# Kernel tuning notes

Hardware: AMD Instinct MI355X
Metric: run time of the kernel (lower is better)

The kernel has to match this reference:

```python
import jax, jax.numpy as jnp
import numpy as np

K = 20            # neighbors
C = 21            # num_classes
P = 16            # patch_size
NROWS = 14        # img_size // patch_size
H = NROWS * P     # 224
TEMP = 1.0        # temperature


def setup_inputs() -> dict:
    key = jax.random.key(0)
    k1, k2, k3 = jax.random.split(key, 3)
    test_feature = jax.random.normal(k1, (8, 196, 384), dtype=jnp.float32)
    train_features = jax.random.normal(k2, (384, 50000), dtype=jnp.float32)
    train_labels = jax.random.randint(k3, (256, 50000), 0, C, dtype=jnp.int32)
    return {"test_feature": test_feature, "train_features": train_features,
            "train_labels": train_labels}


def reference(test_feature, train_features, train_labels):
    bs = test_feature.shape[0]
    # similarity: [bs, num_patches, N_train]
    sim = jnp.einsum('bpd,dn->bpn', test_feature, train_features)
    sim_k, idx = jax.lax.top_k(sim, K)              # [bs, 196, K]
    # gather neighbor patch labels: train_labels [P^2, N] -> [bs, 196, K, P^2]
    nb = train_labels.T[idx]
    # make_grid with nrow=NROWS, padding=0: assemble patches into [bs, K, H, H]
    nb = nb.reshape(bs, NROWS, NROWS, K, P, P)
    nb = nb.transpose(0, 3, 1, 4, 2, 5).reshape(bs, K, H, H)
    nb = nb.transpose(0, 2, 3, 1)                   # [bs, H, H, K]
    # weighted majority vote: nearest-upsample similarities 14x14 -> 224x224
    w = sim_k.reshape(bs, NROWS, NROWS, K)
    w = jnp.repeat(jnp.repeat(w, P, axis=1), P, axis=2)   # [bs, H, H, K]
    w = jax.nn.softmax(w / TEMP, axis=-1)
    # one-hot vote expressed as scatter-add over classes (same math, no
    # [bs,H,H,K,C] materialization)
    rows = jnp.arange(bs * H * H)
    vote = jnp.zeros((bs * H * H, C), dtype=w.dtype)
    vote = vote.at[rows[:, None], nb.reshape(bs * H * H, K)].add(
        w.reshape(bs * H * H, K))
    vote = vote.reshape(bs, H, H, C)
    pred = jnp.argmax(vote, axis=-1)                # [bs, H, H] int
    return pred
```

## Files before the change

kernel.cpp:

```cpp
#include <hip/hip_runtime.h>
#include <float.h>

#define N_TRAIN 50000
#define NPAD    50176
#define NBLK    392
#define MPAD    1664
#define DDIM    384
#define M_ROWS  1568
#define KNN     20
#define K2      24
#define SELMAX  64
#define NCLS    21
#define CAPBUF  768
#define CBMAX   256

typedef __attribute__((ext_vector_type(8))) short bf16x8;
typedef __attribute__((ext_vector_type(4))) float f32x4;

#define GLOAD_LDS16(gp, lp) \
  __builtin_amdgcn_global_load_lds((const __attribute__((address_space(1))) void*)(gp), \
                                   (__attribute__((address_space(3))) void*)(lp), 16, 0, 0)

static __device__ __forceinline__ unsigned short f2bf(float f) {
  unsigned int u = __float_as_uint(f);
  unsigned int r = (u + 0x7fffu + ((u >> 16) & 1u)) >> 16;
  return (unsigned short)r;
}
static __device__ __forceinline__ unsigned int flip32(unsigned int u) {
  return (u & 0x80000000u) ? ~u : (u | 0x80000000u);
}

__global__ __launch_bounds__(256) void transpose_labels(const int* __restrict__ labels,
                                                        unsigned char* __restrict__ labT) {
  __shared__ int tile[64][65];
  const int t  = threadIdx.x;
  const int c0 = blockIdx.x * 64;
  const int r0 = blockIdx.y * 64;
#pragma unroll
  for (int i = 0; i < 16; ++i) {
    int idx = i * 256 + t;
    int r = idx >> 6, c = idx & 63;
    int cc = c0 + c;
    tile[r][c] = (cc < N_TRAIN) ? labels[(size_t)(r0 + r) * N_TRAIN + cc] : 0;
  }
  __syncthreads();
#pragma unroll
  for (int i = 0; i < 16; ++i) {
    int idx = i * 256 + t;
    int c = idx >> 6, r = idx & 63;
    int cc = c0 + c;
    if (cc < N_TRAIN) labT[(size_t)cc * 256 + r0 + r] = (unsigned char)tile[r][c];
  }
}

__global__ __launch_bounds__(256) void conv_bf16A(const float* __restrict__ test,
                                                  unsigned short* __restrict__ bf16A) {
  int idx = blockIdx.x * 256 + threadIdx.x;
  if (idx >= MPAD * DDIM) return;
  int row = idx / DDIM;
  bf16A[idx] = (row < M_ROWS) ? f2bf(test[idx]) : (unsigned short)0;
}

__global__ __launch_bounds__(256) void trans_train_fused(const float* __restrict__ train,
                                                         unsigned short* __restrict__ bhT,
                                                         float* __restrict__ trainT) {
  __shared__ float tile[64][65];
  const int t  = threadIdx.x;
  const int c0 = blockIdx.x * 64;
  const int r0 = blockIdx.y * 64;
#pragma unroll
  for (int i = 0; i < 16; ++i) {
    int idx = i * 256 + t;
    int r = idx >> 6, c = idx & 63;
    int cc = c0 + c;
    tile[r][c] = (cc < N_TRAIN) ? train[(size_t)(r0 + r) * N_TRAIN + cc] : 0.f;
  }
  __syncthreads();
#pragma unroll
  for (int i = 0; i < 16; ++i) {
    int idx = i * 256 + t;
    int c = idx >> 6, r = idx & 63;
    int cc = c0 + c;
    float v = tile[r][c];
    bhT[(size_t)cc * DDIM + r0 + r] = f2bf(v);
    if (cc < N_TRAIN) trainT[(size_t)cc * DDIM + r0 + r] = v;
  }
}

__global__ __launch_bounds__(256) void mfma_gemm(const unsigned short* __restrict__ bf16A,
                                                 const unsigned short* __restrict__ bhT,
                                                 unsigned short* __restrict__ keybuf,
                                                 unsigned short* __restrict__ blkmax) {
  __shared__ unsigned short lds[16384];
  const int t = threadIdx.x;

  const int flat = blockIdx.x;
  const int wrk  = (flat & 7) * 637 + (flat >> 3);
  const int nblk = wrk / 13, mblk = wrk % 13;
  const int m0 = mblk * 128, n0 = nblk * 128;

  const int wid = t >> 6, lane = t & 63;
  const int wr = wid >> 1, wc = wid & 1;
  const int l15 = lane & 15, l4 = lane >> 4;
  const int srow  = lane >> 3;
  const int sslot = (lane & 7) ^ srow;

  f32x4 acc[4][4];
  const f32x4 zero = {0.f, 0.f, 0.f, 0.f};
#pragma unroll
  for (int f = 0; f < 4; ++f)
#pragma unroll
    for (int n = 0; n < 4; ++n) acc[f][n] = zero;

  for (int ks = 0; ks < DDIM / 64; ++ks) {
    __syncthreads();
#pragma unroll
    for (int j = 0; j < 4; ++j) {
      int seg  = wid * 4 + j;
      int arow = seg * 8 + srow;
      GLOAD_LDS16(bf16A + (size_t)(m0 + arow) * DDIM + ks * 64 + sslot * 8,
                  &lds[seg * 512]);
      GLOAD_LDS16(bhT + (size_t)(n0 + arow) * DDIM + ks * 64 + sslot * 8,
                  &lds[8192 + seg * 512]);
    }
    __syncthreads();
#pragma unroll
    for (int k2 = 0; k2 < 2; ++k2) {
      bf16x8 a[4], b[4];
#pragma unroll
      for (int f = 0; f < 4; ++f) {
        int row = wr * 64 + f * 16 + l15;
        int kel = (k2 * 32 + l4 * 8) ^ ((row & 7) << 3);
        a[f] = *(bf16x8*)&lds[row * 64 + kel];
      }
#pragma unroll
      for (int n = 0; n < 4; ++n) {
        int row = wc * 64 + n * 16 + l15;
        int kel = (k2 * 32 + l4 * 8) ^ ((row & 7) << 3);
        b[n] = *(bf16x8*)&lds[8192 + row * 64 + kel];
      }
#pragma unroll
      for (int f = 0; f < 4; ++f)
#pragma unroll
        for (int n = 0; n < 4; ++n)
          acc[f][n] = __builtin_amdgcn_mfma_f32_16x16x32_bf16(a[f], b[n], acc[f][n], 0, 0, 0);
    }
  }

  __syncthreads();
#pragma unroll
  for (int f = 0; f < 4; ++f) {
#pragma unroll
    for (int n = 0; n < 4; ++n) {
      const int col = wc * 64 + n * 16 + l15;
#pragma unroll
      for (int r = 0; r < 4; ++r) {
        const int row = wr * 64 + f * 16 + l4 * 4 + r;
        unsigned int k16 = flip32(__float_as_uint(acc[f][n][r])) >> 16;
        lds[row * 128 + (col ^ ((row & 15) << 3))] = (unsigned short)k16;
      }
    }
  }
  __syncthreads();

  const bool boundary = (n0 + 128 > N_TRAIN);
#pragma unroll
  for (int i = 0; i < 8; ++i) {
    int idx = i * 256 + t;
    int row = idx >> 4;
    int c8  = (idx & 15) * 8;
    uint4 v = *(uint4*)&lds[row * 128 + (c8 ^ ((row & 15) << 3))];
    if (boundary) {
      int nv = N_TRAIN - (n0 + c8);
      v.x &= ((0 < nv) ? 0x0000FFFFu : 0u) | ((1 < nv) ? 0xFFFF0000u : 0u);
      v.y &= ((2 < nv) ? 0x0000FFFFu : 0u) | ((3 < nv) ? 0xFFFF0000u : 0u);
      v.z &= ((4 < nv) ? 0x0000FFFFu : 0u) | ((5 < nv) ? 0xFFFF0000u : 0u);
      v.w &= ((6 < nv) ? 0x0000FFFFu : 0u) | ((7 < nv) ? 0xFFFF0000u : 0u);
    }
    unsigned int mx = v.x & 0xFFFFu;
    mx = max(mx, v.x >> 16); mx = max(mx, v.y & 0xFFFFu); mx = max(mx, v.y >> 16);
    mx = max(mx, v.z & 0xFFFFu); mx = max(mx, v.z >> 16);
    mx = max(mx, v.w & 0xFFFFu); mx = max(mx, v.w >> 16);
    mx = max(mx, (unsigned int)__shfl_xor((int)mx, 1));
    mx = max(mx, (unsigned int)__shfl_xor((int)mx, 2));
    mx = max(mx, (unsigned int)__shfl_xor((int)mx, 4));
    mx = max(mx, (unsigned int)__shfl_xor((int)mx, 8));
    if ((lane & 15) == 0) blkmax[(size_t)(m0 + row) * NBLK + nblk] = (unsigned short)mx;
    if (m0 + row < M_ROWS)
      *(uint4*)&keybuf[(size_t)(m0 + row) * NPAD + n0 + c8] = v;
  }
}

__global__ __launch_bounds__(256) void select_all(const unsigned short* __restrict__ keybuf,
                                                  const unsigned short* __restrict__ blkmax,
                                                  int* __restrict__ selCols,
                                                  int* __restrict__ selCnt) {
  const int t = threadIdx.x, m = blockIdx.x;
  __shared__ unsigned short bm[NBLK];
  __shared__ int clist[CBMAX];
  __shared__ int ccnt;
  __shared__ unsigned int smax[256];
  __shared__ unsigned int sbuf[CAPBUF];
  __shared__ short srk[CAPBUF];
  __shared__ unsigned int scnt, sTauA, sTau;
  __shared__ int sC2;

  if (t == 0) { ccnt = 0; scnt = 0u; sC2 = 0; }
  for (int i = t; i < NBLK; i += 256) bm[i] = blkmax[(size_t)m * NBLK + i];
  __syncthreads();

  for (int i = t; i < NBLK; i += 256) {
    unsigned short v = bm[i];
    int cgt = 0;
    for (int j = 0; j < NBLK; ++j) cgt += (bm[j] > v) ? 1 : 0;
    if (cgt < K2) { int p = atomicAdd(&ccnt, 1); if (p < CBMAX) clist[p] = i; }
  }
  __syncthreads();
  const int CB = min(ccnt, CBMAX);
  const int TOT = CB * 128;

  unsigned int tmx = 0u;
  for (int i = t; i < TOT; i += 256) {
    int col = clist[i >> 7] * 128 + (i & 127);
    unsigned int k = keybuf[(size_t)m * NPAD + col];
    if (k > tmx) tmx = k;
  }
  smax[t] = (tmx << 8) | (unsigned int)(255 - t);
  __syncthreads();
  {
    unsigned int myc = smax[t];
    int rnk = 0;
    for (int j = 0; j < 256; ++j) rnk += (smax[j] > myc) ? 1 : 0;
    if (rnk == K2 - 1) sTauA = myc >> 8;
  }
  __syncthreads();
  const unsigned int tauB = sTauA;

  for (int i = t; i < TOT; i += 256) {
    int col = clist[i >> 7] * 128 + (i & 127);
    unsigned int k = keybuf[(size_t)m * NPAD + col];
    if (k >= tauB) {
      unsigned int p = atomicAdd(&scnt, 1u);
      if (p < CAPBUF) sbuf[p] = (k << 16) | (unsigned int)(0xFFFF - col);
    }
  }
  __syncthreads();
  const int C = (int)min(scnt, (unsigned int)CAPBUF);

  for (int s = t; s < C; s += 256) {
    unsigned int e = sbuf[s];
    int rk = 0;
    for (int j = 0; j < C; ++j) rk += (sbuf[j] > e) ? 1 : 0;
    srk[s] = (short)rk;
    if (rk == K2 - 1) sTau = e >> 16;
  }
  __syncthreads();
  const unsigned int tau = sTau;
  for (int s = t; s < C; s += 256) {
    unsigned int e = sbuf[s];
    int rk = (int)srk[s];
    if ((e >> 16) >= tau && rk < SELMAX) {
      selCols[(size_t)m * SELMAX + rk] = 0xFFFF - (int)(e & 0xFFFFu);
      atomicMax(&sC2, rk + 1);
    }
  }
  __syncthreads();
  if (t == 0) selCnt[m] = sC2 < SELMAX ? sC2 : SELMAX;
}

__global__ __launch_bounds__(256) void refine_softmax(const int* __restrict__ selCols,
                                                      const int* __restrict__ selCnt,
                                                      const float* __restrict__ test,
                                                      const float* __restrict__ trainT,
                                                      double* __restrict__ wval,
                                                      int* __restrict__ widx) {
  const int m = blockIdx.x, t = threadIdx.x;
  __shared__ int    sIdx[SELMAX];
  __shared__ double rvs[SELMAX];
  __shared__ double sv2[SELMAX];
  __shared__ int    si2[SELMAX];
  __shared__ double earr[KNN];
  const int C2 = selCnt[m];
  if (t < C2) sIdx[t] = selCols[(size_t)m * SELMAX + t];
  __syncthreads();

  const int wid = t >> 6, lane = t & 63;
  float tr[DDIM / 64];
#pragma unroll
  for (int dd = 0; dd < DDIM / 64; ++dd)
    tr[dd] = test[(size_t)m * DDIM + dd * 64 + lane];
#pragma unroll 1
  for (int c = wid; c < C2; c += 4) {
    const float* Tc = trainT + (size_t)sIdx[c] * DDIM;
    double s = 0.0;
#pragma unroll
    for (int dd = 0; dd < DDIM / 64; ++dd)
      s += (double)tr[dd] * (double)Tc[dd * 64 + lane];
#pragma unroll
    for (int off = 32; off > 0; off >>= 1) s += __shfl_xor(s, off);
    if (lane == 0) rvs[c] = s;
  }
  __syncthreads();

  if (t < C2) {
    double v = rvs[t]; int id = sIdx[t];
    int r = 0;
    for (int n = 0; n < C2; ++n)
      r += (rvs[n] > v || (rvs[n] == v && sIdx[n] < id)) ? 1 : 0;
    sv2[r] = v; si2[r] = id;
  }
  __syncthreads();

  if (t < KNN) earr[t] = exp(sv2[t] - sv2[0]);
  __syncthreads();
  if (t < KNN) {
    double ssum = 0.0;
    for (int k = 0; k < KNN; ++k) ssum += earr[k];
    wval[(size_t)m * KNN + t] = earr[t] / ssum;
    widx[(size_t)m * KNN + t] = si2[t];
  }
}

__global__ __launch_bounds__(256) void vote_kernel(const double* __restrict__ wval,
                                                   const int* __restrict__ widx,
                                                   const unsigned char* __restrict__ labT,
                                                   int* __restrict__ out) {
  const int m = blockIdx.x, t = threadIdx.x;
  __shared__ double sw[KNN];
  __shared__ int    si[KNN];
  if (t < KNN) { sw[t] = wval[(size_t)m * KNN + t]; si[t] = widx[(size_t)m * KNN + t]; }
  __syncthreads();

  unsigned int packed[5];
#pragma unroll
  for (int q = 0; q < 5; ++q) {
    unsigned int p = 0;
#pragma unroll
    for (int j = 0; j < 4; ++j)
      p |= (unsigned int)labT[(size_t)si[q * 4 + j] * 256 + t] << (8 * j);
    packed[q] = p;
  }

  double best = -1.0; int bc = 0;
#pragma unroll 1
  for (int c = 0; c < NCLS; ++c) {
    double s = 0.0;
#pragma unroll
    for (int k = 0; k < KNN; ++k) {
      unsigned int lab = (packed[k >> 2] >> ((k & 3) * 8)) & 255u;
      s += (lab == (unsigned int)c) ? sw[k] : 0.0;
    }
    if (s > best) { best = s; bc = c; }
  }

  const int b = m / 196, p = m % 196;
  const int py = p / 14, px = p % 14;
  const int i = t >> 4, j = t & 15;
  out[((size_t)b * 224 + py * 16 + i) * 224 + px * 16 + j] = bc;
}

extern "C" void kernel_launch(void* const* d_in, const int* in_sizes, int n_in,
                              void* d_out, int out_size, void* d_ws, size_t ws_size,
                              hipStream_t stream) {
  const float* test  = (const float*)d_in[0];
  const float* train = (const float*)d_in[1];
  const int* labels  = (const int*)d_in[2];
  int* out = (int*)d_out;
  char* ws = (char*)d_ws;

  unsigned char*  labT    = (unsigned char*)ws;
  unsigned short* bf16A   = (unsigned short*)(ws + 12800000);
  unsigned short* bhT     = (unsigned short*)(ws + 14077952);
  unsigned short* keybuf  = (unsigned short*)(ws + 52613120);
  float*          trainT  = (float*)(ws + 209965056);
  unsigned short* blkmax  = (unsigned short*)(ws + 286765056);
  int*            selCols = (int*)(ws + 288069632);
  int*            selCnt  = (int*)(ws + 288471040);
  double*         wval    = (double*)(ws + 288477312);
  int*            widx    = (int*)(ws + 288728192);

  transpose_labels<<<dim3(782, 4), 256, 0, stream>>>(labels, labT);
  conv_bf16A<<<dim3((MPAD * DDIM + 255) / 256), 256, 0, stream>>>(test, bf16A);
  trans_train_fused<<<dim3(784, 6), 256, 0, stream>>>(train, bhT, trainT);
  mfma_gemm<<<dim3(13 * NBLK), 256, 0, stream>>>(bf16A, bhT, keybuf, blkmax);
  select_all<<<dim3(M_ROWS), 256, 0, stream>>>(keybuf, blkmax, selCols, selCnt);
  refine_softmax<<<dim3(M_ROWS), 256, 0, stream>>>(selCols, selCnt, test, trainT, wval, widx);
  vote_kernel<<<dim3(M_ROWS), 256, 0, stream>>>(wval, widx, labT, out);
}
```

Measured before the change: 259.8 us.

## Enlarge GEMM tiles with double-buffered LDS pipeline and fuse tail kernels

The similarity GEMM moves from 128x128 tiles with 256 threads to 256x256 tiles with 512 threads. K-slices are double-buffered in 128KB of dynamic LDS, with explicit vmcnt waits and setprio around the MFMA block. The goal is more data reuse per block and overlap of global loads with MFMA work. The select, refine and vote kernels are fused into one tail kernel, which removes two launches and the global round-trips for selected columns and weights. The risks are lower occupancy, since the large LDS footprint allows only about two blocks per CU, and padding M to 1792, which adds wasted rows.

```diff
diff --git a/kernel.cpp b/kernel.cpp
--- a/kernel.cpp
+++ b/kernel.cpp
@@ -4,7 +4,8 @@
 #define N_TRAIN 50000
 #define NPAD    50176
 #define NBLK    392
-#define MPAD    1664
+#define NBLK2   196
+#define MPAD    1792
 #define DDIM    384
 #define M_ROWS  1568
 #define KNN     20
@@ -20,6 +21,7 @@
 #define GLOAD_LDS16(gp, lp) \
   __builtin_amdgcn_global_load_lds((const __attribute__((address_space(1))) void*)(gp), \
                                    (__attribute__((address_space(3))) void*)(lp), 16, 0, 0)
+#define WAITVM(N) asm volatile("s_waitcnt vmcnt(" #N ")" ::: "memory")
 
 static __device__ __forceinline__ unsigned short f2bf(float f) {
   unsigned int u = __float_as_uint(f);
@@ -87,89 +89,106 @@
   }
 }
 
-__global__ __launch_bounds__(256) void mfma_gemm(const unsigned short* __restrict__ bf16A,
-                                                 const unsigned short* __restrict__ bhT,
-                                                 unsigned short* __restrict__ keybuf,
-                                                 unsigned short* __restrict__ blkmax) {
-  __shared__ unsigned short lds[16384];
+__global__ __launch_bounds__(512, 2) void mfma_gemm(const unsigned short* __restrict__ bf16A,
+                                                    const unsigned short* __restrict__ bhT,
+                                                    unsigned short* __restrict__ keybuf,
+                                                    unsigned short* __restrict__ blkmax) {
+  extern __shared__ unsigned short lds16[];
   const int t = threadIdx.x;
 
   const int flat = blockIdx.x;
-  const int wrk  = (flat & 7) * 637 + (flat >> 3);
-  const int nblk = wrk / 13, mblk = wrk % 13;
-  const int m0 = mblk * 128, n0 = nblk * 128;
+  const int xcd = flat & 7, jj = flat >> 3;
+  const int wg = (xcd < 4 ? xcd * 172 : 688 + (xcd - 4) * 171) + jj;
+  const int mblk = wg % 7, nblk = wg / 7;
+  const int m0 = mblk * 256, n0 = nblk * 256;
 
   const int wid = t >> 6, lane = t & 63;
-  const int wr = wid >> 1, wc = wid & 1;
+  const int wr = wid >> 2, wc = wid & 3;
   const int l15 = lane & 15, l4 = lane >> 4;
-  const int srow  = lane >> 3;
-  const int sslot = (lane & 7) ^ srow;
-
-  f32x4 acc[4][4];
+  const int srow = t >> 3;
+  const int sx   = (t & 7) ^ (srow & 7);
+
+  f32x4 acc[8][4];
   const f32x4 zero = {0.f, 0.f, 0.f, 0.f};
 #pragma unroll
-  for (int f = 0; f < 4; ++f)
+  for (int f = 0; f < 8; ++f)
 #pragma unroll
     for (int n = 0; n < 4; ++n) acc[f][n] = zero;
 
-  for (int ks = 0; ks < DDIM / 64; ++ks) {
-    __syncthreads();
-#pragma unroll
-    for (int j = 0; j < 4; ++j) {
-      int seg  = wid * 4 + j;
-      int arow = seg * 8 + srow;
-      GLOAD_LDS16(bf16A + (size_t)(m0 + arow) * DDIM + ks * 64 + sslot * 8,
-                  &lds[seg * 512]);
-      GLOAD_LDS16(bhT + (size_t)(n0 + arow) * DDIM + ks * 64 + sslot * 8,
-                  &lds[8192 + seg * 512]);
-    }
-    __syncthreads();
-#pragma unroll
-    for (int k2 = 0; k2 < 2; ++k2) {
-      bf16x8 a[4], b[4];
-#pragma unroll
-      for (int f = 0; f < 4; ++f) {
-        int row = wr * 64 + f * 16 + l15;
-        int kel = (k2 * 32 + l4 * 8) ^ ((row & 7) << 3);
-        a[f] = *(bf16x8*)&lds[row * 64 + kel];
-      }
-#pragma unroll
-      for (int n = 0; n < 4; ++n) {
-        int row = wc * 64 + n * 16 + l15;
-        int kel = (k2 * 32 + l4 * 8) ^ ((row & 7) << 3);
-        b[n] = *(bf16x8*)&lds[8192 + row * 64 + kel];
-      }
-#pragma unroll
-      for (int f = 0; f < 4; ++f)
-#pragma unroll
-        for (int n = 0; n < 4; ++n)
-          acc[f][n] = __builtin_amdgcn_mfma_f32_16x16x32_bf16(a[f], b[n], acc[f][n], 0, 0, 0);
-    }
-  }
-
-  __syncthreads();
-#pragma unroll
-  for (int f = 0; f < 4; ++f) {
+#define STAGE_HALF(tk, h)                                                          \
+  {                                                                                \
+    const int slot_ = (tk) & 1;                                                    \
+    _Pragma("unroll")                                                              \
+    for (int j2 = 2 * (h); j2 < 2 * (h) + 2; ++j2) {                               \
+      GLOAD_LDS16(bf16A + (size_t)(m0 + j2 * 64 + srow) * DDIM + (tk) * 64 + sx * 8, \
+                  &lds16[slot_ * 16384 + j2 * 4096 + wid * 512]);                  \
+      GLOAD_LDS16(bhT + (size_t)(n0 + j2 * 64 + srow) * DDIM + (tk) * 64 + sx * 8, \
+                  &lds16[32768 + slot_ * 16384 + j2 * 4096 + wid * 512]);          \
+    }                                                                              \
+  }
+
+  STAGE_HALF(0, 0);
+  STAGE_HALF(0, 1);
+
+#pragma unroll
+  for (int p = 0; p < 12; ++p) {
+    const int tk = p >> 1, h = p & 1;
+    if (tk + 1 < 6) STAGE_HALF(tk + 1, h);
+    if (p >= 10)      { WAITVM(0); }
+    else if (h == 0)  { WAITVM(4); }
+    else              { WAITVM(8); }
+    __builtin_amdgcn_s_barrier();
+    asm volatile("" ::: "memory");
+
+    const int aBase = (tk & 1) * 16384;
+    const int bBase = 32768 + (tk & 1) * 16384;
+    const int physc = ((h * 4 + l4) ^ (l15 & 7)) * 8;
+    bf16x8 a[8], b[4];
+#pragma unroll
+    for (int f = 0; f < 8; ++f)
+      a[f] = *(const bf16x8*)&lds16[aBase + (wr * 128 + f * 16 + l15) * 64 + physc];
+#pragma unroll
+    for (int n = 0; n < 4; ++n)
+      b[n] = *(const bf16x8*)&lds16[bBase + (wc * 64 + n * 16 + l15) * 64 + physc];
+
+    __builtin_amdgcn_s_setprio(1);
+#pragma unroll
+    for (int f = 0; f < 8; ++f)
+#pragma unroll
+      for (int n = 0; n < 4; ++n)
+        acc[f][n] = __builtin_amdgcn_mfma_f32_16x16x32_bf16(a[f], b[n], acc[f][n], 0, 0, 0);
+    __builtin_amdgcn_s_setprio(0);
+
+    asm volatile("s_waitcnt lgkmcnt(0)" ::: "memory");
+    __builtin_amdgcn_s_barrier();
+  }
+
+  __syncthreads();
+#pragma unroll
+  for (int f = 0; f < 8; ++f) {
+    const int row0 = wr * 128 + f * 16 + l4 * 4;
 #pragma unroll
     for (int n = 0; n < 4; ++n) {
       const int col = wc * 64 + n * 16 + l15;
+      const int cl = col >> 3, ce = col & 7;
 #pragma unroll
       for (int r = 0; r < 4; ++r) {
-        const int row = wr * 64 + f * 16 + l4 * 4 + r;
+        const int rr = row0 + r;
         unsigned int k16 = flip32(__float_as_uint(acc[f][n][r])) >> 16;
-        lds[row * 128 + (col ^ ((row & 15) << 3))] = (unsigned short)k16;
+        lds16[rr * 256 + ((cl ^ (rr & 31)) << 3) + ce] = (unsigned short)k16;
       }
     }
   }
   __syncthreads();
 
-  const bool boundary = (n0 + 128 > N_TRAIN);
-#pragma unroll
-  for (int i = 0; i < 8; ++i) {
-    int idx = i * 256 + t;
-    int row = idx >> 4;
-    int c8  = (idx & 15) * 8;
-    uint4 v = *(uint4*)&lds[row * 128 + (c8 ^ ((row & 15) << 3))];
+  const bool boundary = (n0 + 256 > N_TRAIN);
+#pragma unroll
+  for (int i = 0; i < 16; ++i) {
+    int idx = i * 512 + t;
+    int row = idx >> 5;
+    int cL  = idx & 31;
+    uint4 v = *(uint4*)&lds16[row * 256 + ((cL ^ (row & 31)) << 3)];
+    int c8 = cL * 8;
     if (boundary) {
       int nv = N_TRAIN - (n0 + c8);
       v.x &= ((0 < nv) ? 0x0000FFFFu : 0u) | ((1 < nv) ? 0xFFFF0000u : 0u);
@@ -185,16 +204,24 @@
     mx = max(mx, (unsigned int)__shfl_xor((int)mx, 2));
     mx = max(mx, (unsigned int)__shfl_xor((int)mx, 4));
     mx = max(mx, (unsigned int)__shfl_xor((int)mx, 8));
-    if ((lane & 15) == 0) blkmax[(size_t)(m0 + row) * NBLK + nblk] = (unsigned short)mx;
-    if (m0 + row < M_ROWS)
-      *(uint4*)&keybuf[(size_t)(m0 + row) * NPAD + n0 + c8] = v;
-  }
-}
-
-__global__ __launch_bounds__(256) void select_all(const unsigned short* __restrict__ keybuf,
+    const int grow = m0 + row;
+    if (grow < M_ROWS) {
+      if ((lane & 15) == 0) {
+        int half = (lane >> 4) & 1;
+        blkmax[(size_t)grow * NBLK + nblk * 2 + half] = (unsigned short)mx;
+      }
+      *(uint4*)&keybuf[(size_t)grow * NPAD + n0 + c8] = v;
+    }
+  }
+#undef STAGE_HALF
+}
+
+__global__ __launch_bounds__(256) void tail_fused(const unsigned short* __restrict__ keybuf,
                                                   const unsigned short* __restrict__ blkmax,
-                                                  int* __restrict__ selCols,
-                                                  int* __restrict__ selCnt) {
+                                                  const float* __restrict__ test,
+                                                  const float* __restrict__ trainT,
+                                                  const unsigned char* __restrict__ labT,
+                                                  int* __restrict__ out) {
   const int t = threadIdx.x, m = blockIdx.x;
   __shared__ unsigned short bm[NBLK];
   __shared__ int clist[CBMAX];
@@ -204,6 +231,13 @@
   __shared__ short srk[CAPBUF];
   __shared__ unsigned int scnt, sTauA, sTau;
   __shared__ int sC2;
+  __shared__ int selC[SELMAX];
+  __shared__ double rvs[SELMAX];
+  __shared__ double sv2[SELMAX];
+  __shared__ int    si2[SELMAX];
+  __shared__ double earr[KNN];
+  __shared__ double wv[KNN];
+  __shared__ int    wi[KNN];
 
   if (t == 0) { ccnt = 0; scnt = 0u; sC2 = 0; }
   for (int i = t; i < NBLK; i += 256) bm[i] = blkmax[(size_t)m * NBLK + i];
@@ -260,29 +294,12 @@
     unsigned int e = sbuf[s];
     int rk = (int)srk[s];
     if ((e >> 16) >= tau && rk < SELMAX) {
-      selCols[(size_t)m * SELMAX + rk] = 0xFFFF - (int)(e & 0xFFFFu);
+      selC[rk] = 0xFFFF - (int)(e & 0xFFFFu);
       atomicMax(&sC2, rk + 1);
     }
   }
   __syncthreads();
-  if (t == 0) selCnt[m] = sC2 < SELMAX ? sC2 : SELMAX;
-}
-
-__global__ __launch_bounds__(256) void refine_softmax(const int* __restrict__ selCols,
-                                                      const int* __restrict__ selCnt,
-                                                      const float* __restrict__ test,
-                                                      const float* __restrict__ trainT,
-                                                      double* __restrict__ wval,
-                                                      int* __restrict__ widx) {
-  const int m = blockIdx.x, t = threadIdx.x;
-  __shared__ int    sIdx[SELMAX];
-  __shared__ double rvs[SELMAX];
-  __shared__ double sv2[SELMAX];
-  __shared__ int    si2[SELMAX];
-  __shared__ double earr[KNN];
-  const int C2 = selCnt[m];
-  if (t < C2) sIdx[t] = selCols[(size_t)m * SELMAX + t];
-  __syncthreads();
+  const int C2 = sC2 < SELMAX ? sC2 : SELMAX;
 
   const int wid = t >> 6, lane = t & 63;
   float tr[DDIM / 64];
@@ -291,7 +308,7 @@
     tr[dd] = test[(size_t)m * DDIM + dd * 64 + lane];
 #pragma unroll 1
   for (int c = wid; c < C2; c += 4) {
-    const float* Tc = trainT + (size_t)sIdx[c] * DDIM;
+    const float* Tc = trainT + (size_t)selC[c] * DDIM;
     double s = 0.0;
 #pragma unroll
     for (int dd = 0; dd < DDIM / 64; ++dd)
@@ -303,10 +320,10 @@
   __syncthreads();
 
   if (t < C2) {
-    double v = rvs[t]; int id = sIdx[t];
+    double v = rvs[t]; int id = selC[t];
     int r = 0;
     for (int n = 0; n < C2; ++n)
-      r += (rvs[n] > v || (rvs[n] == v && sIdx[n] < id)) ? 1 : 0;
+      r += (rvs[n] > v || (rvs[n] == v && selC[n] < id)) ? 1 : 0;
     sv2[r] = v; si2[r] = id;
   }
   __syncthreads();
@@ -316,19 +333,9 @@
   if (t < KNN) {
     double ssum = 0.0;
     for (int k = 0; k < KNN; ++k) ssum += earr[k];
-    wval[(size_t)m * KNN + t] = earr[t] / ssum;
-    widx[(size_t)m * KNN + t] = si2[t];
-  }
-}
-
-__global__ __launch_bounds__(256) void vote_kernel(const double* __restrict__ wval,
-                                                   const int* __restrict__ widx,
-                                                   const unsigned char* __restrict__ labT,
-                                                   int* __restrict__ out) {
-  const int m = blockIdx.x, t = threadIdx.x;
-  __shared__ double sw[KNN];
-  __shared__ int    si[KNN];
-  if (t < KNN) { sw[t] = wval[(size_t)m * KNN + t]; si[t] = widx[(size_t)m * KNN + t]; }
+    wv[t] = earr[t] / ssum;
+    wi[t] = si2[t];
+  }
   __syncthreads();
 
   unsigned int packed[5];
@@ -337,10 +344,9 @@
     unsigned int p = 0;
 #pragma unroll
     for (int j = 0; j < 4; ++j)
-      p |= (unsigned int)labT[(size_t)si[q * 4 + j] * 256 + t] << (8 * j);
+      p |= (unsigned int)labT[(size_t)wi[q * 4 + j] * 256 + t] << (8 * j);
     packed[q] = p;
   }
-
   double best = -1.0; int bc = 0;
 #pragma unroll 1
   for (int c = 0; c < NCLS; ++c) {
@@ -348,11 +354,10 @@
 #pragma unroll
     for (int k = 0; k < KNN; ++k) {
       unsigned int lab = (packed[k >> 2] >> ((k & 3) * 8)) & 255u;
-      s += (lab == (unsigned int)c) ? sw[k] : 0.0;
+      s += (lab == (unsigned int)c) ? wv[k] : 0.0;
     }
     if (s > best) { best = s; bc = c; }
   }
-
   const int b = m / 196, p = m % 196;
   const int py = p / 14, px = p % 14;
   const int i = t >> 4, j = t & 15;
@@ -370,20 +375,14 @@
 
   unsigned char*  labT    = (unsigned char*)ws;
   unsigned short* bf16A   = (unsigned short*)(ws + 12800000);
-  unsigned short* bhT     = (unsigned short*)(ws + 14077952);
-  unsigned short* keybuf  = (unsigned short*)(ws + 52613120);
-  float*          trainT  = (float*)(ws + 209965056);
-  unsigned short* blkmax  = (unsigned short*)(ws + 286765056);
-  int*            selCols = (int*)(ws + 288069632);
-  int*            selCnt  = (int*)(ws + 288471040);
-  double*         wval    = (double*)(ws + 288477312);
-  int*            widx    = (int*)(ws + 288728192);
+  unsigned short* bhT     = (unsigned short*)(ws + 14176256);
+  unsigned short* keybuf  = (unsigned short*)(ws + 52711424);
+  float*          trainT  = (float*)(ws + 210063360);
+  unsigned short* blkmax  = (unsigned short*)(ws + 286863360);
 
   transpose_labels<<<dim3(782, 4), 256, 0, stream>>>(labels, labT);
   conv_bf16A<<<dim3((MPAD * DDIM + 255) / 256), 256, 0, stream>>>(test, bf16A);
   trans_train_fused<<<dim3(784, 6), 256, 0, stream>>>(train, bhT, trainT);
-  mfma_gemm<<<dim3(13 * NBLK), 256, 0, stream>>>(bf16A, bhT, keybuf, blkmax);
-  select_all<<<dim3(M_ROWS), 256, 0, stream>>>(keybuf, blkmax, selCols, selCnt);
-  refine_softmax<<<dim3(M_ROWS), 256, 0, stream>>>(selCols, selCnt, test, trainT, wval, widx);
-  vote_kernel<<<dim3(M_ROWS), 256, 0, stream>>>(wval, widx, labT, out);
-}
+  mfma_gemm<<<dim3(7 * NBLK2), 512, 131072, stream>>>(bf16A, bhT, keybuf, blkmax);
+  tail_fused<<<dim3(M_ROWS), 256, 0, stream>>>(keybuf, blkmax, test, trainT, labT, out);
+}
```

Result: no change. 261.0 us (+0.5%).
